# Performance work log

Hardware: AMD Instinct MI355X
Metric: run time of the kernel (lower is better)

## Reference

```python
import jax, jax.numpy as jnp
import numpy as np

N_KERNELS = 5
MUL_FACTOR = 2.0
# 2.0 ** (arange(5) - 2) = [0.25, 0.5, 1, 2, 4]
BANDWIDTH_MULTIPLIERS = MUL_FACTOR ** (np.arange(N_KERNELS) - N_KERNELS // 2)


def setup_inputs() -> dict:
    key = jax.random.key(0)
    kx, ky = jax.random.split(key)
    X = jax.random.normal(kx, (4096, 256), dtype=jnp.float32)
    Y = jax.random.normal(ky, (4096, 256), dtype=jnp.float32)
    return {"X": X, "Y": Y}


def _pairwise_sq_dists(Z):
    # ||z_i - z_j||^2 via GEMM; clamp tiny negatives from roundoff.
    sq = jnp.sum(Z * Z, axis=-1)  # [2N]
    d2 = sq[:, None] + sq[None, :] - 2.0 * (Z @ Z.T)  # [2N, 2N]
    return jnp.maximum(d2, 0.0)


def reference(X, Y):
    n = X.shape[0]
    Z = jnp.concatenate([X, Y], axis=0)  # [2N, D]
    d2 = _pairwise_sq_dists(Z)  # [2N, 2N]
    n_samples = d2.shape[0]
    # bandwidth uses .data in torch -> detached
    bandwidth = jax.lax.stop_gradient(d2.sum()) / (n_samples ** 2 - n_samples)
    mults = jnp.asarray(BANDWIDTH_MULTIPLIERS, dtype=d2.dtype)  # [5]
    # K = sum_k exp(-d2 / (bandwidth * mult_k))
    K = jnp.exp(-d2[None, :, :] / (bandwidth * mults)[:, None, None]).sum(axis=0)
    XX = K[:n, :n].mean()
    XY = K[:n, n:].mean()
    YY = K[n:, n:].mean()
    return XX - 2.0 * XY + YY
```

## Files before the change

### kernel.cpp

```cpp
#include <hip/hip_runtime.h>
#include <math.h>


#define N_HALF 4096
#define DIM 256
#define M_TOT 8192
#define TILE 128
#define NT 64
#define NT_HALF 32
#define NCHUNK 512

typedef unsigned short ushort_t;
typedef __attribute__((ext_vector_type(8))) short short8;
typedef __attribute__((ext_vector_type(4))) float floatx4;

__device__ ushort_t g_zf[M_TOT * DIM];

__device__ __forceinline__ ushort_t f2bf(float f) {
    unsigned u = __float_as_uint(f);
    u += 0x7fffu + ((u >> 16) & 1u);
    return (ushort_t)(u >> 16);
}

__device__ __forceinline__ void gload_lds16(const ushort_t* g, ushort_t* l) {
    __builtin_amdgcn_global_load_lds(
        (const __attribute__((address_space(1))) void*)g,
        (__attribute__((address_space(3))) void*)l, 16, 0, 0);
}

__device__ __forceinline__ void stage1(const ushort_t* gA, const ushort_t* gB,
                                       int kk, ushort_t* buf, int wave, int lane) {
#pragma unroll
    for (int i = 0; i < 2; ++i) {
        const int c = wave * 2 + i;
        gload_lds16(gA + (size_t)c * 4096 + kk * 512 + lane * 8, buf + c * 512);
        gload_lds16(gB + (size_t)c * 4096 + kk * 512 + lane * 8, buf + 4096 + c * 512);
    }
}

__global__ __launch_bounds__(256) void k_prep(const float* __restrict__ X,
                                              const float* __restrict__ Y,
                                              float* __restrict__ sq,
                                              float* __restrict__ colsum_r,
                                              float* __restrict__ Ssum_r) {
    __shared__ float cpart[4][256];
    __shared__ float spart[4];
    const int t = threadIdx.x, wave = t >> 6, lane = t & 63;
    const int row0 = blockIdx.x * 16 + wave * 4;
    const int kk = lane >> 3, q = (lane >> 1) & 3, j0 = (lane & 1) * 4;
    float c0 = 0.f, c1 = 0.f, c2 = 0.f, c3 = 0.f, ssum = 0.f;
#pragma unroll
    for (int i = 0; i < 4; ++i) {
        const int row = row0 + i;
        const float* p = (row < N_HALF) ? (X + (size_t)row * DIM)
                                        : (Y + (size_t)(row - N_HALF) * DIM);
        const float4 v = *((const float4*)p + lane);
        ushort4 hi;
        hi.x = f2bf(v.x); hi.y = f2bf(v.y); hi.z = f2bf(v.z); hi.w = f2bf(v.w);
        const int rb = row >> 4, m = row & 15;
        *(ushort4*)(g_zf + (size_t)rb * 4096 + kk * 512 + q * 128 + m * 8 + j0) = hi;
        c0 += v.x; c1 += v.y; c2 += v.z; c3 += v.w;
        float s = fmaf(v.x, v.x, fmaf(v.y, v.y, fmaf(v.z, v.z, v.w * v.w)));
#pragma unroll
        for (int off = 32; off > 0; off >>= 1) s += __shfl_xor(s, off);
        if (lane == 0) sq[row] = s;
        ssum += s;
    }
    float4 cp; cp.x = c0; cp.y = c1; cp.z = c2; cp.w = c3;
    *(float4*)&cpart[wave][lane * 4] = cp;
    if (lane == 0) spart[wave] = ssum;
    __syncthreads();
    const float cs = cpart[0][t] + cpart[1][t] + cpart[2][t] + cpart[3][t];
    const int rep = blockIdx.x & 7;
    atomicAdd(&colsum_r[rep * 256 + t], cs);
    if (t == 0) atomicAdd(&Ssum_r[rep], spart[0] + spart[1] + spart[2] + spart[3]);
}

__global__ __launch_bounds__(256) void k_bw(const float* __restrict__ colsum_r,
                                            const float* __restrict__ Ssum_r,
                                            float* __restrict__ c2out) {
    __shared__ double sred[4];
    const int t = threadIdx.x, lane = t & 63, wave = t >> 6;
    float csf = 0.f;
#pragma unroll
    for (int r = 0; r < 8; ++r) csf += colsum_r[r * 256 + t];
    double p = (double)csf * (double)csf;
#pragma unroll
    for (int off = 32; off > 0; off >>= 1) p += __shfl_xor(p, off);
    if (lane == 0) sred[wave] = p;
    __syncthreads();
    if (t == 0) {
        const double SS = sred[0] + sred[1] + sred[2] + sred[3];
        float Sf = 0.f;
#pragma unroll
        for (int r = 0; r < 8; ++r) Sf += Ssum_r[r];
        const double sum_d2 = 2.0 * (double)M_TOT * (double)Sf - 2.0 * SS;
        const double bw = sum_d2 / ((double)M_TOT * (double)M_TOT - (double)M_TOT);
        c2out[0] = (float)(1.4426950408889634 / (4.0 * bw));
    }
}

__global__ __launch_bounds__(256, 2) void k_gram(const float* __restrict__ sq,
                                                 const float* __restrict__ c2p,
                                                 double* __restrict__ acc,
                                                 unsigned* __restrict__ cnt,
                                                 float* __restrict__ out) {
    __shared__ __attribute__((aligned(16))) ushort_t lds[4][8192];
    __shared__ double redw[4][3];

    const int bid = (int)blockIdx.x;
    const int cc = (bid & 7) * 64 + (bid >> 3);
    const int nst = ((cc & 15) == 0) ? 5 : 4;
    const int f0 = cc * 4 + ((cc + 15) >> 4);

    const int t = threadIdx.x;
    const int lane = t & 63, wave = t >> 6;
    const int l15 = lane & 15, quad = lane >> 4;
    const int wrow = (wave >> 1) * 64, wcol = (wave & 1) * 64;
    const int a0 = (wave >> 1) * 4, b0 = (wave & 1) * 4;
    const int laneoff = quad * 128 + l15 * 8;

    const float c2 = c2p[0];
    const float twoc2 = 2.f * c2;

    int ti = (int)((129.0f - sqrtf(16641.0f - 8.0f * (float)f0)) * 0.5f);
    if (ti < 0) ti = 0; if (ti > NT - 1) ti = NT - 1;
    while (ti * NT - ti * (ti - 1) / 2 > f0) --ti;
    while ((ti + 1) * NT - (ti + 1) * ti / 2 <= f0) ++ti;
    int tj = ti + (f0 - (ti * NT - ti * (ti - 1) / 2));

    int s_ti = ti, s_tj = tj, s_kk = 0;
    const ushort_t* sgA = g_zf + (size_t)s_ti * 32768;
    const ushort_t* sgB = g_zf + (size_t)s_tj * 32768;
#define ADV_STAGE() do { if (++s_kk == 8) { s_kk = 0; ++s_tj;                 \
        if (s_tj == NT) { ++s_ti; s_tj = s_ti; }                              \
        sgA = g_zf + (size_t)s_ti * 32768;                                    \
        sgB = g_zf + (size_t)s_tj * 32768; } } while (0)

#pragma unroll
    for (int p = 0; p < 3; ++p) {
        stage1(sgA, sgB, s_kk, lds[p], wave, lane);
        ADV_STAGE();
    }

    double lxx = 0.0, lxy = 0.0, lyy = 0.0;

#pragma unroll 1
    for (int s = 0; s < nst; ++s) {
        const bool last = (s == nst - 1);

        floatx4 accv[4][4];
#pragma unroll
        for (int mi = 0; mi < 4; ++mi)
#pragma unroll
            for (int ni = 0; ni < 4; ++ni) accv[mi][ni] = (floatx4)0.f;

#pragma unroll
        for (int kkc = 0; kkc < 8; ++kkc) {
            if (last && kkc == 6)      asm volatile("s_waitcnt vmcnt(4)" ::: "memory");
            else if (last && kkc == 7) asm volatile("s_waitcnt vmcnt(0)" ::: "memory");
            else                       asm volatile("s_waitcnt vmcnt(8)" ::: "memory");
            __builtin_amdgcn_s_barrier();
            __builtin_amdgcn_sched_barrier(0);

            const ushort_t* lA = lds[kkc & 3];
            const ushort_t* lB = lds[kkc & 3] + 4096;
            short8 af[4], bf[4];
#pragma unroll
            for (int mi = 0; mi < 4; ++mi)
                af[mi] = *(const short8*)(lA + (a0 + mi) * 512 + laneoff);
#pragma unroll
            for (int ni = 0; ni < 4; ++ni)
                bf[ni] = *(const short8*)(lB + (b0 + ni) * 512 + laneoff);

            if (!last || kkc < 5) {
                stage1(sgA, sgB, s_kk, lds[(kkc + 3) & 3], wave, lane);
                ADV_STAGE();
            }

            __builtin_amdgcn_s_setprio(1);
#pragma unroll
            for (int mi = 0; mi < 4; ++mi)
#pragma unroll
                for (int ni = 0; ni < 4; ++ni)
                    accv[mi][ni] = __builtin_amdgcn_mfma_f32_16x16x32_bf16(
                        af[mi], bf[ni], accv[mi][ni], 0, 0, 0);
            __builtin_amdgcn_s_setprio(0);
        }

        const int arow0 = ti * TILE, brow0 = tj * TILE;
        float nsj[4];
#pragma unroll
        for (int ni = 0; ni < 4; ++ni)
            nsj[ni] = -c2 * sq[brow0 + wcol + ni * 16 + l15];
        floatx4 nsi4[4];
#pragma unroll
        for (int mi = 0; mi < 4; ++mi) {
            const float4 sv = *(const float4*)&sq[arow0 + wrow + mi * 16 + quad * 4];
            nsi4[mi][0] = -c2 * sv.x; nsi4[mi][1] = -c2 * sv.y;
            nsi4[mi][2] = -c2 * sv.z; nsi4[mi][3] = -c2 * sv.w;
        }
        floatx4 sum4 = (floatx4)0.f;
#pragma unroll
        for (int mi = 0; mi < 4; ++mi) {
#pragma unroll
            for (int ni = 0; ni < 4; ++ni) {
                const floatx4 addv = nsi4[mi] + (floatx4)nsj[ni];
                floatx4 arg = twoc2 * accv[mi][ni] + addv;
                floatx4 tt;
#pragma unroll
                for (int r = 0; r < 4; ++r) tt[r] = exp2f(fminf(arg[r], 0.f));
                const floatx4 t2 = tt * tt, t4 = t2 * t2, t8 = t4 * t4, t16 = t8 * t8;
                sum4 += (tt + t2) + (t4 + t8) + t16;
            }
        }
        const float fsum = (sum4[0] + sum4[1]) + (sum4[2] + sum4[3]);
        const double contrib = ((ti == tj) ? 1.0 : 2.0) * (double)fsum;
        if (tj < NT_HALF)       lxx += contrib;
        else if (ti < NT_HALF)  lxy += contrib;
        else                    lyy += contrib;

        ++tj; if (tj == NT) { ++ti; tj = ti; }
    }
#undef ADV_STAGE

#pragma unroll
    for (int off = 32; off > 0; off >>= 1) {
        lxx += __shfl_xor(lxx, off);
        lxy += __shfl_xor(lxy, off);
        lyy += __shfl_xor(lyy, off);
    }
    if (lane == 0) { redw[wave][0] = lxx; redw[wave][1] = lxy; redw[wave][2] = lyy; }
    __syncthreads();
    if (t == 0) {
        double sxx = 0.0, sxy = 0.0, syy = 0.0;
#pragma unroll
        for (int wv = 0; wv < 4; ++wv) {
            sxx += redw[wv][0]; sxy += redw[wv][1]; syy += redw[wv][2];
        }
        if (sxx != 0.0) atomicAdd(&acc[0], sxx);
        if (sxy != 0.0) atomicAdd(&acc[1], sxy);
        if (syy != 0.0) atomicAdd(&acc[2], syy);
        __threadfence();
        const unsigned old = atomicAdd(cnt, 1u);
        if (old == (0xAAAAAAAAu + (unsigned)(NCHUNK - 1)) ||
            old == (unsigned)(NCHUNK - 1)) {
            const double xx = atomicAdd(&acc[0], 0.0);
            const double xy = atomicAdd(&acc[1], 0.0);
            const double yy = atomicAdd(&acc[2], 0.0);
            out[0] = (float)((xx + yy - xy) *
                             (1.0 / ((double)N_HALF * (double)N_HALF)));
        }
    }
}

extern "C" void kernel_launch(void* const* d_in, const int* in_sizes, int n_in,
                              void* d_out, int out_size, void* d_ws, size_t ws_size,
                              hipStream_t stream) {
    const float* X = (const float*)d_in[0];
    const float* Y = (const float*)d_in[1];
    char* ws = (char*)d_ws;
    float* sq        = (float*)ws;
    float* colsum_r  = (float*)(ws + 32768);
    float* Ssum_r    = (float*)(ws + 40960);
    unsigned* cnt    = (unsigned*)(ws + 40992);
    double* acc      = (double*)(ws + 41000);
    float* c2ws      = (float*)(ws + 41024);
    float* out = (float*)d_out;

    hipLaunchKernelGGL(k_prep, dim3(512), dim3(256), 0, stream,
                       X, Y, sq, colsum_r, Ssum_r);
    hipLaunchKernelGGL(k_bw, dim3(1), dim3(256), 0, stream,
                       colsum_r, Ssum_r, c2ws);
    hipLaunchKernelGGL(k_gram, dim3(NCHUNK), dim3(256), 0, stream,
                       sq, c2ws, acc, cnt, out);
}
```

Before: 113.8 us.

## Keep A-tile MFMA operands in registers and stream only B through LDS

Each wave now loads its full A-row fragments (4 row blocks × 8 k-chunks) into registers once per row tile. It reloads them only when the row tile index changes. Only the B tile is staged through LDS with global_load_lds, which halves the LDS footprint and the per-step global-to-LDS traffic, and the vmcnt wait thresholds are adjusted to match. The cost is about 128 extra VGPRs per lane, which raises register pressure and risks spills or lower occupancy under launch_bounds(256,2). The A reloads are also plain global loads that are not overlapped with the compute pipeline.

Result: no change. 115.8 us (+1.7%).

```diff
diff --git a/kernel.cpp b/kernel.cpp
--- a/kernel.cpp
+++ b/kernel.cpp
@@ -28,13 +28,12 @@
         (__attribute__((address_space(3))) void*)l, 16, 0, 0);
 }
 
-__device__ __forceinline__ void stage1(const ushort_t* gA, const ushort_t* gB,
-                                       int kk, ushort_t* buf, int wave, int lane) {
+__device__ __forceinline__ void stageB(const ushort_t* gB, int kk,
+                                       ushort_t* buf, int wave, int lane) {
 #pragma unroll
     for (int i = 0; i < 2; ++i) {
         const int c = wave * 2 + i;
-        gload_lds16(gA + (size_t)c * 4096 + kk * 512 + lane * 8, buf + c * 512);
-        gload_lds16(gB + (size_t)c * 4096 + kk * 512 + lane * 8, buf + 4096 + c * 512);
+        gload_lds16(gB + (size_t)c * 4096 + kk * 512 + lane * 8, buf + c * 512);
     }
 }
 
@@ -105,7 +104,7 @@
                                                  double* __restrict__ acc,
                                                  unsigned* __restrict__ cnt,
                                                  float* __restrict__ out) {
-    __shared__ __attribute__((aligned(16))) ushort_t lds[4][8192];
+    __shared__ __attribute__((aligned(16))) ushort_t lds[4][4096];
     __shared__ double redw[4][3];
 
     const int bid = (int)blockIdx.x;
@@ -117,7 +116,7 @@
     const int lane = t & 63, wave = t >> 6;
     const int l15 = lane & 15, quad = lane >> 4;
     const int wrow = (wave >> 1) * 64, wcol = (wave & 1) * 64;
-    const int a0 = (wave >> 1) * 4, b0 = (wave & 1) * 4;
+    const int b0 = (wave & 1) * 4;
     const int laneoff = quad * 128 + l15 * 8;
 
     const float c2 = c2p[0];
@@ -129,17 +128,26 @@
     while ((ti + 1) * NT - (ti + 1) * ti / 2 <= f0) ++ti;
     int tj = ti + (f0 - (ti * NT - ti * (ti - 1) / 2));
 
+    short8 aR[4][8];
+    {
+        const ushort_t* aBase =
+            g_zf + (size_t)(ti * 8 + (wave >> 1) * 4) * 4096 + laneoff;
+#pragma unroll
+        for (int mi = 0; mi < 4; ++mi)
+#pragma unroll
+            for (int kk = 0; kk < 8; ++kk)
+                aR[mi][kk] = *(const short8*)(aBase + (size_t)mi * 4096 + kk * 512);
+    }
+
     int s_ti = ti, s_tj = tj, s_kk = 0;
-    const ushort_t* sgA = g_zf + (size_t)s_ti * 32768;
     const ushort_t* sgB = g_zf + (size_t)s_tj * 32768;
 #define ADV_STAGE() do { if (++s_kk == 8) { s_kk = 0; ++s_tj;                 \
         if (s_tj == NT) { ++s_ti; s_tj = s_ti; }                              \
-        sgA = g_zf + (size_t)s_ti * 32768;                                    \
         sgB = g_zf + (size_t)s_tj * 32768; } } while (0)
 
 #pragma unroll
     for (int p = 0; p < 3; ++p) {
-        stage1(sgA, sgB, s_kk, lds[p], wave, lane);
+        stageB(sgB, s_kk, lds[p], wave, lane);
         ADV_STAGE();
     }
 
@@ -157,24 +165,20 @@
 
 #pragma unroll
         for (int kkc = 0; kkc < 8; ++kkc) {
-            if (last && kkc == 6)      asm volatile("s_waitcnt vmcnt(4)" ::: "memory");
+            if (last && kkc == 6)      asm volatile("s_waitcnt vmcnt(2)" ::: "memory");
             else if (last && kkc == 7) asm volatile("s_waitcnt vmcnt(0)" ::: "memory");
-            else                       asm volatile("s_waitcnt vmcnt(8)" ::: "memory");
+            else                       asm volatile("s_waitcnt vmcnt(4)" ::: "memory");
             __builtin_amdgcn_s_barrier();
             __builtin_amdgcn_sched_barrier(0);
 
-            const ushort_t* lA = lds[kkc & 3];
-            const ushort_t* lB = lds[kkc & 3] + 4096;
-            short8 af[4], bf[4];
-#pragma unroll
-            for (int mi = 0; mi < 4; ++mi)
-                af[mi] = *(const short8*)(lA + (a0 + mi) * 512 + laneoff);
+            const ushort_t* lB = lds[kkc & 3];
+            short8 bf[4];
 #pragma unroll
             for (int ni = 0; ni < 4; ++ni)
                 bf[ni] = *(const short8*)(lB + (b0 + ni) * 512 + laneoff);
 
             if (!last || kkc < 5) {
-                stage1(sgA, sgB, s_kk, lds[(kkc + 3) & 3], wave, lane);
+                stageB(sgB, s_kk, lds[(kkc + 3) & 3], wave, lane);
                 ADV_STAGE();
             }
 
@@ -184,7 +188,7 @@
 #pragma unroll
                 for (int ni = 0; ni < 4; ++ni)
                     accv[mi][ni] = __builtin_amdgcn_mfma_f32_16x16x32_bf16(
-                        af[mi], bf[ni], accv[mi][ni], 0, 0, 0);
+                        aR[mi][kkc], bf[ni], accv[mi][ni], 0, 0, 0);
             __builtin_amdgcn_s_setprio(0);
         }
 
@@ -220,7 +224,17 @@
         else if (ti < NT_HALF)  lxy += contrib;
         else                    lyy += contrib;
 
+        const int pti = ti;
         ++tj; if (tj == NT) { ++ti; tj = ti; }
+        if (!last && ti != pti) {
+            const ushort_t* aBase =
+                g_zf + (size_t)(ti * 8 + (wave >> 1) * 4) * 4096 + laneoff;
+#pragma unroll
+            for (int mi = 0; mi < 4; ++mi)
+#pragma unroll
+                for (int kk = 0; kk < 8; ++kk)
+                    aR[mi][kk] = *(const short8*)(aBase + (size_t)mi * 4096 + kk * 512);
+        }
     }
 #undef ADV_STAGE
 
```

## Double-buffer LDS fragment registers and deepen global prefetch to four stages

Applied to the files above, without the earlier changes.

The K-loop now loads the A/B MFMA fragments for the next k-chunk from LDS into a second register set while the current chunk's MFMAs run, instead of reading LDS and then computing in sequence. The global-to-LDS prefetch distance grows from three to four stages, and the vmcnt/lgkmcnt wait schedule is reworked to match the new buffer rotation. The aim is to hide LDS read latency and global load latency behind matrix math. The cost is more live registers, which may lower occupancy, and a more fragile wait schedule.

Result: faster. 111.5 us (-2.0%).

```diff
diff --git a/kernel.cpp b/kernel.cpp
--- a/kernel.cpp
+++ b/kernel.cpp
@@ -138,16 +138,28 @@
         sgB = g_zf + (size_t)s_tj * 32768; } } while (0)
 
 #pragma unroll
-    for (int p = 0; p < 3; ++p) {
+    for (int p = 0; p < 4; ++p) {
         stage1(sgA, sgB, s_kk, lds[p], wave, lane);
         ADV_STAGE();
     }
+    asm volatile("s_waitcnt vmcnt(12)" ::: "memory");
+    __builtin_amdgcn_s_barrier();
+    __builtin_amdgcn_sched_barrier(0);
+
+    short8 af0[4], bf0[4], af1[4], bf1[4];
+#pragma unroll
+    for (int mi = 0; mi < 4; ++mi)
+        af0[mi] = *(const short8*)(lds[0] + (a0 + mi) * 512 + laneoff);
+#pragma unroll
+    for (int ni = 0; ni < 4; ++ni)
+        bf0[ni] = *(const short8*)(lds[0] + 4096 + (b0 + ni) * 512 + laneoff);
 
     double lxx = 0.0, lxy = 0.0, lyy = 0.0;
 
 #pragma unroll 1
     for (int s = 0; s < nst; ++s) {
-        const bool last = (s == nst - 1);
+        const bool lastT = (s == nst - 1);
+        const bool firstT = (s == 0);
 
         floatx4 accv[4][4];
 #pragma unroll
@@ -157,36 +169,62 @@
 
 #pragma unroll
         for (int kkc = 0; kkc < 8; ++kkc) {
-            if (last && kkc == 6)      asm volatile("s_waitcnt vmcnt(4)" ::: "memory");
-            else if (last && kkc == 7) asm volatile("s_waitcnt vmcnt(0)" ::: "memory");
-            else                       asm volatile("s_waitcnt vmcnt(8)" ::: "memory");
+            if (lastT && kkc == 5)
+                asm volatile("s_waitcnt vmcnt(4) lgkmcnt(0)" ::: "memory");
+            else if (lastT && kkc >= 6)
+                asm volatile("s_waitcnt vmcnt(0) lgkmcnt(0)" ::: "memory");
+            else if (!firstT && kkc <= 2)
+                asm volatile("s_waitcnt vmcnt(16) lgkmcnt(0)" ::: "memory");
+            else
+                asm volatile("s_waitcnt vmcnt(8) lgkmcnt(0)" ::: "memory");
             __builtin_amdgcn_s_barrier();
             __builtin_amdgcn_sched_barrier(0);
 
-            const ushort_t* lA = lds[kkc & 3];
-            const ushort_t* lB = lds[kkc & 3] + 4096;
-            short8 af[4], bf[4];
-#pragma unroll
-            for (int mi = 0; mi < 4; ++mi)
-                af[mi] = *(const short8*)(lA + (a0 + mi) * 512 + laneoff);
-#pragma unroll
-            for (int ni = 0; ni < 4; ++ni)
-                bf[ni] = *(const short8*)(lB + (b0 + ni) * 512 + laneoff);
-
-            if (!last || kkc < 5) {
-                stage1(sgA, sgB, s_kk, lds[(kkc + 3) & 3], wave, lane);
+            if (!(lastT && kkc == 7)) {
+                const ushort_t* nA = lds[(kkc + 1) & 3];
+                const ushort_t* nB = nA + 4096;
+                if ((kkc & 1) == 0) {
+#pragma unroll
+                    for (int mi = 0; mi < 4; ++mi)
+                        af1[mi] = *(const short8*)(nA + (a0 + mi) * 512 + laneoff);
+#pragma unroll
+                    for (int ni = 0; ni < 4; ++ni)
+                        bf1[ni] = *(const short8*)(nB + (b0 + ni) * 512 + laneoff);
+                } else {
+#pragma unroll
+                    for (int mi = 0; mi < 4; ++mi)
+                        af0[mi] = *(const short8*)(nA + (a0 + mi) * 512 + laneoff);
+#pragma unroll
+                    for (int ni = 0; ni < 4; ++ni)
+                        bf0[ni] = *(const short8*)(nB + (b0 + ni) * 512 + laneoff);
+                }
+            }
+
+            if (!lastT || kkc <= 3) {
+                stage1(sgA, sgB, s_kk, lds[kkc & 3], wave, lane);
                 ADV_STAGE();
             }
 
             __builtin_amdgcn_s_setprio(1);
-#pragma unroll
-            for (int mi = 0; mi < 4; ++mi)
-#pragma unroll
-                for (int ni = 0; ni < 4; ++ni)
-                    accv[mi][ni] = __builtin_amdgcn_mfma_f32_16x16x32_bf16(
-                        af[mi], bf[ni], accv[mi][ni], 0, 0, 0);
+            if ((kkc & 1) == 0) {
+#pragma unroll
+                for (int mi = 0; mi < 4; ++mi)
+#pragma unroll
+                    for (int ni = 0; ni < 4; ++ni)
+                        accv[mi][ni] = __builtin_amdgcn_mfma_f32_16x16x32_bf16(
+                            af0[mi], bf0[ni], accv[mi][ni], 0, 0, 0);
+            } else {
+#pragma unroll
+                for (int mi = 0; mi < 4; ++mi)
+#pragma unroll
+                    for (int ni = 0; ni < 4; ++ni)
+                        accv[mi][ni] = __builtin_amdgcn_mfma_f32_16x16x32_bf16(
+                            af1[mi], bf1[ni], accv[mi][ni], 0, 0, 0);
+            }
             __builtin_amdgcn_s_setprio(0);
         }
+
+        asm volatile("" ::: "memory");
 
         const int arow0 = ti * TILE, brow0 = tj * TILE;
         float nsj[4];
```

## Stage two K-slices per LDS buffer and fold bandwidth kernel into prep

Applied to the files above, without the earlier changes.

The Gram kernel now loads two 32-wide K slices into each LDS stage buffer. That halves the number of wait/barrier points per tile but doubles LDS use to 128 KB per block. The separate single-block bandwidth kernel is removed. Its reduction now runs in the last-arriving prep block, found through an atomic counter, which saves one launch. The larger LDS footprint likely limits the Gram kernel to one block per CU instead of two. The counter check also assumes a zero or 0xAA-poisoned workspace and is never reset visibly.

Result: slower. 131.3 us (+15.3%).

```diff
diff --git a/kernel.cpp b/kernel.cpp
--- a/kernel.cpp
+++ b/kernel.cpp
@@ -9,6 +9,7 @@
 #define NT 64
 #define NT_HALF 32
 #define NCHUNK 512
+#define NPREP 512
 
 typedef unsigned short ushort_t;
 typedef __attribute__((ext_vector_type(8))) short short8;
@@ -28,13 +29,18 @@
         (__attribute__((address_space(3))) void*)l, 16, 0, 0);
 }
 
-__device__ __forceinline__ void stage1(const ushort_t* gA, const ushort_t* gB,
-                                       int kk, ushort_t* buf, int wave, int lane) {
-#pragma unroll
-    for (int i = 0; i < 2; ++i) {
-        const int c = wave * 2 + i;
-        gload_lds16(gA + (size_t)c * 4096 + kk * 512 + lane * 8, buf + c * 512);
-        gload_lds16(gB + (size_t)c * 4096 + kk * 512 + lane * 8, buf + 4096 + c * 512);
+__device__ __forceinline__ void stage2(const ushort_t* gA, const ushort_t* gB,
+                                       int kk0, ushort_t* buf, int wave, int lane) {
+#pragma unroll
+    for (int s = 0; s < 2; ++s) {
+#pragma unroll
+        for (int i = 0; i < 2; ++i) {
+            const int c = wave * 2 + i;
+            gload_lds16(gA + (size_t)c * 4096 + (kk0 + s) * 512 + lane * 8,
+                        buf + s * 4096 + c * 512);
+            gload_lds16(gB + (size_t)c * 4096 + (kk0 + s) * 512 + lane * 8,
+                        buf + 8192 + s * 4096 + c * 512);
+        }
     }
 }
 
@@ -42,9 +48,13 @@
                                               const float* __restrict__ Y,
                                               float* __restrict__ sq,
                                               float* __restrict__ colsum_r,
-                                              float* __restrict__ Ssum_r) {
+                                              float* __restrict__ Ssum_r,
+                                              unsigned* __restrict__ pcnt,
+                                              float* __restrict__ c2out) {
     __shared__ float cpart[4][256];
     __shared__ float spart[4];
+    __shared__ double sred[4];
+    __shared__ int lastflag;
     const int t = threadIdx.x, wave = t >> 6, lane = t & 63;
     const int row0 = blockIdx.x * 16 + wave * 4;
     const int kk = lane >> 3, q = (lane >> 1) & 3, j0 = (lane & 1) * 4;
@@ -74,29 +84,33 @@
     const int rep = blockIdx.x & 7;
     atomicAdd(&colsum_r[rep * 256 + t], cs);
     if (t == 0) atomicAdd(&Ssum_r[rep], spart[0] + spart[1] + spart[2] + spart[3]);
-}
-
-__global__ __launch_bounds__(256) void k_bw(const float* __restrict__ colsum_r,
-                                            const float* __restrict__ Ssum_r,
-                                            float* __restrict__ c2out) {
-    __shared__ double sred[4];
-    const int t = threadIdx.x, lane = t & 63, wave = t >> 6;
-    float csf = 0.f;
-#pragma unroll
-    for (int r = 0; r < 8; ++r) csf += colsum_r[r * 256 + t];
-    double p = (double)csf * (double)csf;
-#pragma unroll
-    for (int off = 32; off > 0; off >>= 1) p += __shfl_xor(p, off);
-    if (lane == 0) sred[wave] = p;
+
+    if (t == 0) {
+        __threadfence();
+        const unsigned old = atomicAdd(pcnt, 1u);
+        lastflag = (old == (0xAAAAAAAAu + (unsigned)(NPREP - 1)) ||
+                    old == (unsigned)(NPREP - 1)) ? 1 : 0;
+    }
     __syncthreads();
-    if (t == 0) {
-        const double SS = sred[0] + sred[1] + sred[2] + sred[3];
-        float Sf = 0.f;
-#pragma unroll
-        for (int r = 0; r < 8; ++r) Sf += Ssum_r[r];
-        const double sum_d2 = 2.0 * (double)M_TOT * (double)Sf - 2.0 * SS;
-        const double bw = sum_d2 / ((double)M_TOT * (double)M_TOT - (double)M_TOT);
-        c2out[0] = (float)(1.4426950408889634 / (4.0 * bw));
+    if (lastflag) {
+        float csf = 0.f;
+#pragma unroll
+        for (int r = 0; r < 8; ++r) csf += atomicAdd(&colsum_r[r * 256 + t], 0.f);
+        double p = (double)csf * (double)csf;
+#pragma unroll
+        for (int off = 32; off > 0; off >>= 1) p += __shfl_xor(p, off);
+        if (lane == 0) sred[wave] = p;
+        __syncthreads();
+        if (t == 0) {
+            const double SS = sred[0] + sred[1] + sred[2] + sred[3];
+            float Sf = 0.f;
+#pragma unroll
+            for (int r = 0; r < 8; ++r) Sf += atomicAdd(&Ssum_r[r], 0.f);
+            const double sum_d2 = 2.0 * (double)M_TOT * (double)Sf - 2.0 * SS;
+            const double bw =
+                sum_d2 / ((double)M_TOT * (double)M_TOT - (double)M_TOT);
+            c2out[0] = (float)(1.4426950408889634 / (4.0 * bw));
+        }
     }
 }
 
@@ -105,7 +119,7 @@
                                                  double* __restrict__ acc,
                                                  unsigned* __restrict__ cnt,
                                                  float* __restrict__ out) {
-    __shared__ __attribute__((aligned(16))) ushort_t lds[4][8192];
+    __shared__ __attribute__((aligned(16))) ushort_t lds[4][16384];
     __shared__ double redw[4][3];
 
     const int bid = (int)blockIdx.x;
@@ -129,17 +143,17 @@
     while ((ti + 1) * NT - (ti + 1) * ti / 2 <= f0) ++ti;
     int tj = ti + (f0 - (ti * NT - ti * (ti - 1) / 2));
 
-    int s_ti = ti, s_tj = tj, s_kk = 0;
+    int s_ti = ti, s_tj = tj, s_k2 = 0;
     const ushort_t* sgA = g_zf + (size_t)s_ti * 32768;
     const ushort_t* sgB = g_zf + (size_t)s_tj * 32768;
-#define ADV_STAGE() do { if (++s_kk == 8) { s_kk = 0; ++s_tj;                 \
+#define ADV_STAGE() do { if (++s_k2 == 4) { s_k2 = 0; ++s_tj;                 \
         if (s_tj == NT) { ++s_ti; s_tj = s_ti; }                              \
         sgA = g_zf + (size_t)s_ti * 32768;                                    \
         sgB = g_zf + (size_t)s_tj * 32768; } } while (0)
 
 #pragma unroll
     for (int p = 0; p < 3; ++p) {
-        stage1(sgA, sgB, s_kk, lds[p], wave, lane);
+        stage2(sgA, sgB, s_k2 * 2, lds[p], wave, lane);
         ADV_STAGE();
     }
 
@@ -156,36 +170,40 @@
             for (int ni = 0; ni < 4; ++ni) accv[mi][ni] = (floatx4)0.f;
 
 #pragma unroll
-        for (int kkc = 0; kkc < 8; ++kkc) {
-            if (last && kkc == 6)      asm volatile("s_waitcnt vmcnt(4)" ::: "memory");
-            else if (last && kkc == 7) asm volatile("s_waitcnt vmcnt(0)" ::: "memory");
-            else                       asm volatile("s_waitcnt vmcnt(8)" ::: "memory");
+        for (int kk2 = 0; kk2 < 4; ++kk2) {
+            if (last && kk2 == 2)      asm volatile("s_waitcnt vmcnt(8)" ::: "memory");
+            else if (last && kk2 == 3) asm volatile("s_waitcnt vmcnt(0)" ::: "memory");
+            else                       asm volatile("s_waitcnt vmcnt(16)" ::: "memory");
             __builtin_amdgcn_s_barrier();
             __builtin_amdgcn_sched_barrier(0);
 
-            const ushort_t* lA = lds[kkc & 3];
-            const ushort_t* lB = lds[kkc & 3] + 4096;
-            short8 af[4], bf[4];
-#pragma unroll
-            for (int mi = 0; mi < 4; ++mi)
-                af[mi] = *(const short8*)(lA + (a0 + mi) * 512 + laneoff);
-#pragma unroll
-            for (int ni = 0; ni < 4; ++ni)
-                bf[ni] = *(const short8*)(lB + (b0 + ni) * 512 + laneoff);
-
-            if (!last || kkc < 5) {
-                stage1(sgA, sgB, s_kk, lds[(kkc + 3) & 3], wave, lane);
+            const ushort_t* buf = lds[kk2];
+
+            if (!last || kk2 == 0) {
+                stage2(sgA, sgB, s_k2 * 2, lds[(kk2 + 3) & 3], wave, lane);
                 ADV_STAGE();
             }
 
-            __builtin_amdgcn_s_setprio(1);
-#pragma unroll
-            for (int mi = 0; mi < 4; ++mi)
+#pragma unroll
+            for (int sl = 0; sl < 2; ++sl) {
+                const ushort_t* lA = buf + sl * 4096;
+                const ushort_t* lB = buf + 8192 + sl * 4096;
+                short8 af[4], bf[4];
+#pragma unroll
+                for (int mi = 0; mi < 4; ++mi)
+                    af[mi] = *(const short8*)(lA + (a0 + mi) * 512 + laneoff);
 #pragma unroll
                 for (int ni = 0; ni < 4; ++ni)
-                    accv[mi][ni] = __builtin_amdgcn_mfma_f32_16x16x32_bf16(
-                        af[mi], bf[ni], accv[mi][ni], 0, 0, 0);
-            __builtin_amdgcn_s_setprio(0);
+                    bf[ni] = *(const short8*)(lB + (b0 + ni) * 512 + laneoff);
+                __builtin_amdgcn_s_setprio(1);
+#pragma unroll
+                for (int mi = 0; mi < 4; ++mi)
+#pragma unroll
+                    for (int ni = 0; ni < 4; ++ni)
+                        accv[mi][ni] = __builtin_amdgcn_mfma_f32_16x16x32_bf16(
+                            af[mi], bf[ni], accv[mi][ni], 0, 0, 0);
+                __builtin_amdgcn_s_setprio(0);
+            }
         }
 
         const int arow0 = ti * TILE, brow0 = tj * TILE;
@@ -266,12 +284,11 @@
     unsigned* cnt    = (unsigned*)(ws + 40992);
     double* acc      = (double*)(ws + 41000);
     float* c2ws      = (float*)(ws + 41024);
+    unsigned* pcnt   = (unsigned*)(ws + 41028);
     float* out = (float*)d_out;
 
-    hipLaunchKernelGGL(k_prep, dim3(512), dim3(256), 0, stream,
-                       X, Y, sq, colsum_r, Ssum_r);
-    hipLaunchKernelGGL(k_bw, dim3(1), dim3(256), 0, stream,
-                       colsum_r, Ssum_r, c2ws);
+    hipLaunchKernelGGL(k_prep, dim3(NPREP), dim3(256), 0, stream,
+                       X, Y, sq, colsum_r, Ssum_r, pcnt, c2ws);
     hipLaunchKernelGGL(k_gram, dim3(NCHUNK), dim3(256), 0, stream,
                        sq, c2ws, acc, cnt, out);
 }
```
